# Kernel tuning notes

Measured on AMD Instinct MI355X. Metric: run time of the kernel, lower is better.

The kernel has to match this reference:

```python
import jax, jax.numpy as jnp
import numpy as np

EMBED_DIM = 1024
ATTN_DIM = 256
B, NQ, NK = 16, 1, 4096


def setup_inputs() -> dict:
    key = jax.random.key(0)
    ks = jax.random.split(key, 7)
    return {
        "q": jax.random.normal(ks[0], (B, NQ, EMBED_DIM), dtype=jnp.float32),
        "k": jax.random.normal(ks[1], (B, NK, EMBED_DIM), dtype=jnp.float32),
        "v": jax.random.normal(ks[2], (B, NK, EMBED_DIM), dtype=jnp.float32),
        "W_kq": jax.random.normal(ks[3], (EMBED_DIM, ATTN_DIM), dtype=jnp.float32) * (1.0 / np.sqrt(EMBED_DIM)),
        "b_kq": jax.random.normal(ks[4], (ATTN_DIM,), dtype=jnp.float32) * 0.02,
        "W_v": jax.random.normal(ks[5], (EMBED_DIM, EMBED_DIM), dtype=jnp.float32) * (1.0 / np.sqrt(EMBED_DIM)),
        "b_v": jax.random.normal(ks[6], (EMBED_DIM,), dtype=jnp.float32) * 0.02,
    }


def reference(q, k, v, W_kq, b_kq, W_v, b_v):
    # Shared kq projection applied to both q and k (embedding_dim -> attention_dim)
    qp = jnp.einsum("bqd,da->bqa", q, W_kq) + b_kq          # [B, NQ, A]
    kp = jnp.einsum("bkd,da->bka", k, W_kq) + b_kq          # [B, NK, A]
    vp = jnp.einsum("bkd,de->bke", v, W_v) + b_v            # [B, NK, E]
    # scores = q @ k^T / sqrt(attention_dim)  (k.shape[2] after projection)
    scores = jnp.einsum("bqa,bka->bqk", qp, kp) / jnp.sqrt(
        jnp.asarray(kp.shape[2], dtype=qp.dtype))
    attn = jax.nn.softmax(scores, axis=2)                   # [B, NQ, NK]
    out = jnp.einsum("bqk,bke->bqe", attn, vp)              # [B, NQ, E]
    return out.squeeze(1)                                   # [B, E] since NQ == 1
```

## Files before the change

### kernel.cpp

```cpp
#include <hip/hip_runtime.h>

#define ED 1024
#define AD 256
#define BB 16
#define NK 4096
#define NCH 64
#define KCH (NK/NCH)

#define OFF_QP    0
#define OFF_T     4096
#define OFF_WSUM  20480
#define OFF_PART  21504
#define OFF_OV    1070080
#define OFF_OPART 1086464

__global__ void k_qp(const float* __restrict__ q, const float* __restrict__ Wkq,
                     const float* __restrict__ bkq, float* __restrict__ qp) {
    int b = blockIdx.x, cg = blockIdx.y, tid = threadIdx.x;
    int c = cg * 64 + (tid & 63), dg = tid >> 6;
    __shared__ float qsh[ED];
    ((float4*)qsh)[tid] = ((const float4*)(q + b * ED))[tid];
    __syncthreads();
    float acc = 0.f;
    #pragma unroll 8
    for (int d = dg; d < ED; d += 4) acc += qsh[d] * Wkq[(size_t)d * AD + c];
    __shared__ float red[4][64];
    red[dg][tid & 63] = acc;
    __syncthreads();
    if (tid < 64) {
        float s = red[0][tid] + red[1][tid] + red[2][tid] + red[3][tid];
        qp[b * AD + cg * 64 + tid] = s + bkq[cg * 64 + tid];
    }
}

__global__ void k_t(const float* __restrict__ Wkq, const float* __restrict__ qp,
                    float* __restrict__ t) {
    int b = blockIdx.y, dbase = blockIdx.x * 128;
    int tid = threadIdx.x, wave = tid >> 6, lane = tid & 63;
    float4 qv = ((const float4*)(qp + b * AD))[lane];
    for (int r = 0; r < 16; ++r) {
        int d1 = dbase + wave * 32 + r;
        int d2 = d1 + 16;
        float4 w1 = ((const float4*)(Wkq + (size_t)d1 * AD))[lane];
        float4 w2 = ((const float4*)(Wkq + (size_t)d2 * AD))[lane];
        float s1 = w1.x*qv.x + w1.y*qv.y + w1.z*qv.z + w1.w*qv.w;
        float s2 = w2.x*qv.x + w2.y*qv.y + w2.z*qv.z + w2.w*qv.w;
        #pragma unroll
        for (int off = 32; off; off >>= 1) {
            s1 += __shfl_down(s1, off, 64);
            s2 += __shfl_down(s2, off, 64);
        }
        if (lane == 0) { t[b * ED + d1] = s1; t[b * ED + d2] = s2; }
    }
}

__global__ void k_fused(const float* __restrict__ k, const float* __restrict__ v,
                        const float* __restrict__ t, float* __restrict__ partial,
                        float* __restrict__ wsum) {
    int ch = blockIdx.x, b = blockIdx.y;
    int tid = threadIdx.x, wave = tid >> 6, lane = tid & 63;
    const float4* tb = (const float4*)(t + b * ED);
    float4 t0 = tb[lane], t1 = tb[64 + lane], t2 = tb[128 + lane], t3 = tb[192 + lane];
    __shared__ float ash[KCH];
    int row0 = ch * KCH + wave * 16;
    for (int r = 0; r < 8; ++r) {
        const float4* ka = (const float4*)(k + ((size_t)b * NK + row0 + r) * ED);
        const float4* kb = (const float4*)(k + ((size_t)b * NK + row0 + r + 8) * ED);
        float4 a0 = ka[lane], a1 = ka[64 + lane], a2 = ka[128 + lane], a3 = ka[192 + lane];
        float4 b0 = kb[lane], b1 = kb[64 + lane], b2 = kb[128 + lane], b3 = kb[192 + lane];
        float sa = a0.x*t0.x + a0.y*t0.y + a0.z*t0.z + a0.w*t0.w
                 + a1.x*t1.x + a1.y*t1.y + a1.z*t1.z + a1.w*t1.w
                 + a2.x*t2.x + a2.y*t2.y + a2.z*t2.z + a2.w*t2.w
                 + a3.x*t3.x + a3.y*t3.y + a3.z*t3.z + a3.w*t3.w;
        float sb = b0.x*t0.x + b0.y*t0.y + b0.z*t0.z + b0.w*t0.w
                 + b1.x*t1.x + b1.y*t1.y + b1.z*t1.z + b1.w*t1.w
                 + b2.x*t2.x + b2.y*t2.y + b2.z*t2.z + b2.w*t2.w
                 + b3.x*t3.x + b3.y*t3.y + b3.z*t3.z + b3.w*t3.w;
        #pragma unroll
        for (int off = 32; off; off >>= 1) {
            sa += __shfl_down(sa, off, 64);
            sb += __shfl_down(sb, off, 64);
        }
        if (lane == 0) {
            ash[wave * 16 + r]     = __expf(sa * 0.0625f);
            ash[wave * 16 + r + 8] = __expf(sb * 0.0625f);
        }
    }
    __syncthreads();
    if (tid < KCH) {
        float s = ash[tid];
        #pragma unroll
        for (int off = 32; off; off >>= 1) s += __shfl_down(s, off, 64);
        if (tid == 0) wsum[b * NCH + ch] = s;
    }
    const float4* vb = (const float4*)(v + ((size_t)b * NK + (size_t)ch * KCH) * ED);
    float4 acc = {0.f, 0.f, 0.f, 0.f};
    #pragma unroll 8
    for (int kk = 0; kk < KCH; ++kk) {
        float wt = ash[kk];
        float4 vv = vb[(size_t)kk * (ED / 4) + tid];
        acc.x += wt * vv.x; acc.y += wt * vv.y; acc.z += wt * vv.z; acc.w += wt * vv.w;
    }
    ((float4*)partial)[((size_t)(b * NCH + ch)) * (ED / 4) + tid] = acc;
}

__global__ void k_reduce(const float* __restrict__ partial, const float* __restrict__ wsum,
                         float* __restrict__ ov) {
    int b = blockIdx.x, dq = blockIdx.y, tid = threadIdx.x;
    int chg = tid >> 6, c = tid & 63;
    __shared__ float lsh;
    if (tid < 64) {
        float s = wsum[b * NCH + tid];
        #pragma unroll
        for (int off = 32; off; off >>= 1) s += __shfl_down(s, off, 64);
        if (tid == 0) lsh = s;
    }
    const float4* pb = (const float4*)(partial + (size_t)b * NCH * ED);
    float4 s4 = {0.f, 0.f, 0.f, 0.f};
    #pragma unroll 8
    for (int ch = chg; ch < NCH; ch += 4) {
        float4 p = pb[(size_t)ch * (ED / 4) + dq * 64 + c];
        s4.x += p.x; s4.y += p.y; s4.z += p.z; s4.w += p.w;
    }
    __shared__ float4 red[4][64];
    red[chg][c] = s4;
    __syncthreads();
    if (tid < 64) {
        float4 a0 = red[0][tid], a1 = red[1][tid], a2 = red[2][tid], a3 = red[3][tid];
        float linv = 1.0f / lsh;
        float4 r;
        r.x = (a0.x + a1.x + a2.x + a3.x) * linv;
        r.y = (a0.y + a1.y + a2.y + a3.y) * linv;
        r.z = (a0.z + a1.z + a2.z + a3.z) * linv;
        r.w = (a0.w + a1.w + a2.w + a3.w) * linv;
        ((float4*)(ov + b * ED + dq * 256))[tid] = r;
    }
}

__global__ void k_out(const float* __restrict__ ov, const float* __restrict__ Wv,
                      float* __restrict__ opart) {
    int cb = blockIdx.x, dq = blockIdx.y, tid = threadIdx.x;
    int col = cb * 64 + (tid & 63), dg = tid >> 6;
    __shared__ float ovsh[BB][256];
    for (int i = tid; i < BB * 64; i += 256) {
        int bb = i >> 6, c4 = i & 63;
        ((float4*)ovsh[bb])[c4] = ((const float4*)(ov + bb * ED + dq * 256))[c4];
    }
    __syncthreads();
    float acc[BB];
    #pragma unroll
    for (int b = 0; b < BB; ++b) acc[b] = 0.f;
    #pragma unroll 8
    for (int it = 0; it < 64; ++it) {
        int dd = dg + it * 4;
        float w = Wv[(size_t)(dq * 256 + dd) * ED + col];
        #pragma unroll
        for (int b = 0; b < BB; ++b) acc[b] += ovsh[b][dd] * w;
    }
    __shared__ float red[BB][256];
    #pragma unroll
    for (int b = 0; b < BB; ++b) red[b][tid] = acc[b];
    __syncthreads();
    int bgrp = tid >> 6, c = tid & 63;
    #pragma unroll
    for (int bi = 0; bi < 4; ++bi) {
        int b = bgrp * 4 + bi;
        float s = red[b][c] + red[b][64 + c] + red[b][128 + c] + red[b][192 + c];
        opart[((size_t)(dq * BB + b)) * ED + cb * 64 + c] = s;
    }
}

__global__ void k_final(const float* __restrict__ opart, const float* __restrict__ bv,
                        float* __restrict__ out) {
    int b = blockIdx.x, tid = threadIdx.x;
    float4 s = ((const float4*)(opart + (size_t)(0 * BB + b) * ED))[tid];
    #pragma unroll
    for (int dq = 1; dq < 4; ++dq) {
        float4 p = ((const float4*)(opart + (size_t)(dq * BB + b) * ED))[tid];
        s.x += p.x; s.y += p.y; s.z += p.z; s.w += p.w;
    }
    float4 bb = ((const float4*)bv)[tid];
    s.x += bb.x; s.y += bb.y; s.z += bb.z; s.w += bb.w;
    ((float4*)(out + b * ED))[tid] = s;
}

extern "C" void kernel_launch(void* const* d_in, const int* in_sizes, int n_in,
                              void* d_out, int out_size, void* d_ws, size_t ws_size,
                              hipStream_t stream) {
    const float* q   = (const float*)d_in[0];
    const float* k   = (const float*)d_in[1];
    const float* v   = (const float*)d_in[2];
    const float* Wkq = (const float*)d_in[3];
    const float* bkq = (const float*)d_in[4];
    const float* Wv  = (const float*)d_in[5];
    const float* bv  = (const float*)d_in[6];
    float* out = (float*)d_out;
    float* ws  = (float*)d_ws;

    float* qp      = ws + OFF_QP;
    float* t       = ws + OFF_T;
    float* wsum    = ws + OFF_WSUM;
    float* partial = ws + OFF_PART;
    float* ov      = ws + OFF_OV;
    float* opart   = ws + OFF_OPART;

    k_qp    <<<dim3(16, 4),   256, 0, stream>>>(q, Wkq, bkq, qp);
    k_t     <<<dim3(8, 16),   256, 0, stream>>>(Wkq, qp, t);
    k_fused <<<dim3(NCH, BB), 256, 0, stream>>>(k, v, t, partial, wsum);
    k_reduce<<<dim3(16, 4),   256, 0, stream>>>(partial, wsum, ov);
    k_out   <<<dim3(16, 4),   256, 0, stream>>>(ov, Wv, opart);
    k_final <<<16,            256, 0, stream>>>(opart, bv, out);
}
```

Baseline: 175.3 us.

## Stream K and V rows together per wave with register accumulation and LDS reduction

The fused score/value kernel now has each wave read a K row and the matching V row in the same iteration. It computes the score with an xor-shuffle allreduce so every lane holds the weight, then accumulates w*V into per-wave float4 registers. The separate phase that scored all K rows before streaming V is removed, so V loads no longer wait on a block-wide barrier and the two streams can overlap. Per-wave partial sums are combined through a 16KB LDS buffer at the end, which adds register pressure and shared memory that may reduce occupancy.

```diff
diff --git a/kernel.cpp b/kernel.cpp
--- a/kernel.cpp
+++ b/kernel.cpp
@@ -61,47 +61,46 @@
     int tid = threadIdx.x, wave = tid >> 6, lane = tid & 63;
     const float4* tb = (const float4*)(t + b * ED);
     float4 t0 = tb[lane], t1 = tb[64 + lane], t2 = tb[128 + lane], t3 = tb[192 + lane];
-    __shared__ float ash[KCH];
     int row0 = ch * KCH + wave * 16;
-    for (int r = 0; r < 8; ++r) {
-        const float4* ka = (const float4*)(k + ((size_t)b * NK + row0 + r) * ED);
-        const float4* kb = (const float4*)(k + ((size_t)b * NK + row0 + r + 8) * ED);
-        float4 a0 = ka[lane], a1 = ka[64 + lane], a2 = ka[128 + lane], a3 = ka[192 + lane];
-        float4 b0 = kb[lane], b1 = kb[64 + lane], b2 = kb[128 + lane], b3 = kb[192 + lane];
-        float sa = a0.x*t0.x + a0.y*t0.y + a0.z*t0.z + a0.w*t0.w
-                 + a1.x*t1.x + a1.y*t1.y + a1.z*t1.z + a1.w*t1.w
-                 + a2.x*t2.x + a2.y*t2.y + a2.z*t2.z + a2.w*t2.w
-                 + a3.x*t3.x + a3.y*t3.y + a3.z*t3.z + a3.w*t3.w;
-        float sb = b0.x*t0.x + b0.y*t0.y + b0.z*t0.z + b0.w*t0.w
-                 + b1.x*t1.x + b1.y*t1.y + b1.z*t1.z + b1.w*t1.w
-                 + b2.x*t2.x + b2.y*t2.y + b2.z*t2.z + b2.w*t2.w
-                 + b3.x*t3.x + b3.y*t3.y + b3.z*t3.z + b3.w*t3.w;
-        #pragma unroll
-        for (int off = 32; off; off >>= 1) {
-            sa += __shfl_down(sa, off, 64);
-            sb += __shfl_down(sb, off, 64);
-        }
-        if (lane == 0) {
-            ash[wave * 16 + r]     = __expf(sa * 0.0625f);
-            ash[wave * 16 + r + 8] = __expf(sb * 0.0625f);
-        }
-    }
-    __syncthreads();
-    if (tid < KCH) {
-        float s = ash[tid];
-        #pragma unroll
-        for (int off = 32; off; off >>= 1) s += __shfl_down(s, off, 64);
-        if (tid == 0) wsum[b * NCH + ch] = s;
-    }
-    const float4* vb = (const float4*)(v + ((size_t)b * NK + (size_t)ch * KCH) * ED);
-    float4 acc = {0.f, 0.f, 0.f, 0.f};
-    #pragma unroll 8
-    for (int kk = 0; kk < KCH; ++kk) {
-        float wt = ash[kk];
-        float4 vv = vb[(size_t)kk * (ED / 4) + tid];
-        acc.x += wt * vv.x; acc.y += wt * vv.y; acc.z += wt * vv.z; acc.w += wt * vv.w;
-    }
-    ((float4*)partial)[((size_t)(b * NCH + ch)) * (ED / 4) + tid] = acc;
+    const float4* kbase = (const float4*)(k + ((size_t)b * NK + row0) * ED);
+    const float4* vbase = (const float4*)(v + ((size_t)b * NK + row0) * ED);
+    float4 acc0 = {0,0,0,0}, acc1 = {0,0,0,0}, acc2 = {0,0,0,0}, acc3 = {0,0,0,0};
+    float wacc = 0.f;
+    #pragma unroll 2
+    for (int r = 0; r < 16; ++r) {
+        const float4* kr = kbase + (size_t)r * (ED / 4);
+        const float4* vr = vbase + (size_t)r * (ED / 4);
+        float4 k0 = kr[lane], k1 = kr[64 + lane], k2 = kr[128 + lane], k3 = kr[192 + lane];
+        float4 v0 = vr[lane], v1 = vr[64 + lane], v2 = vr[128 + lane], v3 = vr[192 + lane];
+        float s = k0.x*t0.x + k0.y*t0.y + k0.z*t0.z + k0.w*t0.w
+                + k1.x*t1.x + k1.y*t1.y + k1.z*t1.z + k1.w*t1.w
+                + k2.x*t2.x + k2.y*t2.y + k2.z*t2.z + k2.w*t2.w
+                + k3.x*t3.x + k3.y*t3.y + k3.z*t3.z + k3.w*t3.w;
+        #pragma unroll
+        for (int m = 32; m; m >>= 1) s += __shfl_xor(s, m, 64);
+        float w = __expf(s * 0.0625f);
+        wacc += w;
+        acc0.x += w*v0.x; acc0.y += w*v0.y; acc0.z += w*v0.z; acc0.w += w*v0.w;
+        acc1.x += w*v1.x; acc1.y += w*v1.y; acc1.z += w*v1.z; acc1.w += w*v1.w;
+        acc2.x += w*v2.x; acc2.y += w*v2.y; acc2.z += w*v2.z; acc2.w += w*v2.w;
+        acc3.x += w*v3.x; acc3.y += w*v3.y; acc3.z += w*v3.z; acc3.w += w*v3.w;
+    }
+    __shared__ float4 red[4][256];
+    red[wave][lane]       = acc0;
+    red[wave][64 + lane]  = acc1;
+    red[wave][128 + lane] = acc2;
+    red[wave][192 + lane] = acc3;
+    __shared__ float wred[4];
+    if (lane == 0) wred[wave] = wacc;
+    __syncthreads();
+    float4 a0 = red[0][tid], a1 = red[1][tid], a2 = red[2][tid], a3 = red[3][tid];
+    float4 r4;
+    r4.x = a0.x + a1.x + a2.x + a3.x;
+    r4.y = a0.y + a1.y + a2.y + a3.y;
+    r4.z = a0.z + a1.z + a2.z + a3.z;
+    r4.w = a0.w + a1.w + a2.w + a3.w;
+    ((float4*)partial)[((size_t)(b * NCH + ch)) * (ED / 4) + tid] = r4;
+    if (tid == 0) wsum[b * NCH + ch] = wred[0] + wred[1] + wred[2] + wred[3];
 }
 
 __global__ void k_reduce(const float* __restrict__ partial, const float* __restrict__ wsum,
```

After: 171.9 us (median of 2 runs). -2.0%, faster.

## Split fused attention kernel into separate scores and PV kernels with finer row blocks

Applied to the files above, without the earlier changes.

Splits the fused score+weighted-V kernel into a scores kernel that writes unnormalized exp weights and a PV kernel. Each now uses 16-row blocks, so the grid grows from 1024 to 4096 blocks. The larger partial buffer is reduced in two stages. The aim is better memory-level parallelism while streaming K and V. In exchange it adds an extra launch and extra partial-sum traffic.

```diff
diff --git a/kernel.cpp b/kernel.cpp
--- a/kernel.cpp
+++ b/kernel.cpp
@@ -4,15 +4,17 @@
 #define AD 256
 #define BB 16
 #define NK 4096
-#define NCH 64
-#define KCH (NK/NCH)
+#define RPB 16
+#define NBLK (BB * NK / RPB)
 
 #define OFF_QP    0
 #define OFF_T     4096
-#define OFF_WSUM  20480
-#define OFF_PART  21504
-#define OFF_OV    1070080
-#define OFF_OPART 1086464
+#define OFF_W     20480
+#define OFF_WSP   86016
+#define OFF_PART  90112
+#define OFF_PART2 4284416
+#define OFF_OV    4546560
+#define OFF_OPART 4562944
 
 __global__ void k_qp(const float* __restrict__ q, const float* __restrict__ Wkq,
                      const float* __restrict__ bkq, float* __restrict__ qp) {
@@ -54,87 +56,106 @@
     }
 }
 
-__global__ void k_fused(const float* __restrict__ k, const float* __restrict__ v,
-                        const float* __restrict__ t, float* __restrict__ partial,
-                        float* __restrict__ wsum) {
-    int ch = blockIdx.x, b = blockIdx.y;
+__global__ __launch_bounds__(256, 4)
+void k_scores(const float* __restrict__ k, const float* __restrict__ t,
+              float* __restrict__ w, float* __restrict__ wsumPart) {
+    int bid = blockIdx.x;
+    int b = bid >> 8, ch = bid & 255;
     int tid = threadIdx.x, wave = tid >> 6, lane = tid & 63;
     const float4* tb = (const float4*)(t + b * ED);
     float4 t0 = tb[lane], t1 = tb[64 + lane], t2 = tb[128 + lane], t3 = tb[192 + lane];
-    __shared__ float ash[KCH];
-    int row0 = ch * KCH + wave * 16;
-    for (int r = 0; r < 8; ++r) {
-        const float4* ka = (const float4*)(k + ((size_t)b * NK + row0 + r) * ED);
-        const float4* kb = (const float4*)(k + ((size_t)b * NK + row0 + r + 8) * ED);
+    int row0 = ch * RPB + wave * 4;
+    __shared__ float wsh[RPB];
+    #pragma unroll
+    for (int pr = 0; pr < 2; ++pr) {
+        int rA = row0 + pr * 2, rB = rA + 1;
+        const float4* ka = (const float4*)(k + ((size_t)b * NK + rA) * ED);
+        const float4* kb = (const float4*)(k + ((size_t)b * NK + rB) * ED);
         float4 a0 = ka[lane], a1 = ka[64 + lane], a2 = ka[128 + lane], a3 = ka[192 + lane];
-        float4 b0 = kb[lane], b1 = kb[64 + lane], b2 = kb[128 + lane], b3 = kb[192 + lane];
-        float sa = a0.x*t0.x + a0.y*t0.y + a0.z*t0.z + a0.w*t0.w
+        float4 c0 = kb[lane], c1 = kb[64 + lane], c2 = kb[128 + lane], c3 = kb[192 + lane];
+        float sA = a0.x*t0.x + a0.y*t0.y + a0.z*t0.z + a0.w*t0.w
                  + a1.x*t1.x + a1.y*t1.y + a1.z*t1.z + a1.w*t1.w
                  + a2.x*t2.x + a2.y*t2.y + a2.z*t2.z + a2.w*t2.w
                  + a3.x*t3.x + a3.y*t3.y + a3.z*t3.z + a3.w*t3.w;
-        float sb = b0.x*t0.x + b0.y*t0.y + b0.z*t0.z + b0.w*t0.w
-                 + b1.x*t1.x + b1.y*t1.y + b1.z*t1.z + b1.w*t1.w
-                 + b2.x*t2.x + b2.y*t2.y + b2.z*t2.z + b2.w*t2.w
-                 + b3.x*t3.x + b3.y*t3.y + b3.z*t3.z + b3.w*t3.w;
+        float sB = c0.x*t0.x + c0.y*t0.y + c0.z*t0.z + c0.w*t0.w
+                 + c1.x*t1.x + c1.y*t1.y + c1.z*t1.z + c1.w*t1.w
+                 + c2.x*t2.x + c2.y*t2.y + c2.z*t2.z + c2.w*t2.w
+                 + c3.x*t3.x + c3.y*t3.y + c3.z*t3.z + c3.w*t3.w;
         #pragma unroll
-        for (int off = 32; off; off >>= 1) {
-            sa += __shfl_down(sa, off, 64);
-            sb += __shfl_down(sb, off, 64);
+        for (int m = 32; m; m >>= 1) {
+            sA += __shfl_xor(sA, m, 64);
+            sB += __shfl_xor(sB, m, 64);
         }
         if (lane == 0) {
-            ash[wave * 16 + r]     = __expf(sa * 0.0625f);
-            ash[wave * 16 + r + 8] = __expf(sb * 0.0625f);
+            float wA = __expf(sA * 0.0625f), wB = __expf(sB * 0.0625f);
+            w[b * NK + rA] = wA;
+            w[b * NK + rB] = wB;
+            wsh[wave * 4 + pr * 2]     = wA;
+            wsh[wave * 4 + pr * 2 + 1] = wB;
         }
     }
     __syncthreads();
-    if (tid < KCH) {
-        float s = ash[tid];
-        #pragma unroll
-        for (int off = 32; off; off >>= 1) s += __shfl_down(s, off, 64);
-        if (tid == 0) wsum[b * NCH + ch] = s;
-    }
-    const float4* vb = (const float4*)(v + ((size_t)b * NK + (size_t)ch * KCH) * ED);
+    if (wave == 0) {
+        float s = (lane < RPB) ? wsh[lane] : 0.f;
+        s += __shfl_xor(s, 8, 64);
+        s += __shfl_xor(s, 4, 64);
+        s += __shfl_xor(s, 2, 64);
+        s += __shfl_xor(s, 1, 64);
+        if (lane == 0) wsumPart[bid] = s;
+    }
+}
+
+__global__ __launch_bounds__(256, 4)
+void k_pv(const float* __restrict__ v, const float* __restrict__ w,
+          float* __restrict__ partial) {
+    int bid = blockIdx.x;
+    int b = bid >> 8, ch = bid & 255;
+    int tid = threadIdx.x;
+    __shared__ float wsh[RPB];
+    if (tid < RPB) wsh[tid] = w[b * NK + ch * RPB + tid];
+    __syncthreads();
+    const float4* vb = (const float4*)(v + ((size_t)b * NK + (size_t)ch * RPB) * ED);
     float4 acc = {0.f, 0.f, 0.f, 0.f};
-    #pragma unroll 8
-    for (int kk = 0; kk < KCH; ++kk) {
-        float wt = ash[kk];
-        float4 vv = vb[(size_t)kk * (ED / 4) + tid];
+    #pragma unroll
+    for (int r = 0; r < RPB; ++r) {
+        float wt = wsh[r];
+        float4 vv = vb[(size_t)r * (ED / 4) + tid];
         acc.x += wt * vv.x; acc.y += wt * vv.y; acc.z += wt * vv.z; acc.w += wt * vv.w;
     }
-    ((float4*)partial)[((size_t)(b * NCH + ch)) * (ED / 4) + tid] = acc;
-}
-
-__global__ void k_reduce(const float* __restrict__ partial, const float* __restrict__ wsum,
-                         float* __restrict__ ov) {
-    int b = blockIdx.x, dq = blockIdx.y, tid = threadIdx.x;
-    int chg = tid >> 6, c = tid & 63;
-    __shared__ float lsh;
-    if (tid < 64) {
-        float s = wsum[b * NCH + tid];
-        #pragma unroll
-        for (int off = 32; off; off >>= 1) s += __shfl_down(s, off, 64);
-        if (tid == 0) lsh = s;
-    }
-    const float4* pb = (const float4*)(partial + (size_t)b * NCH * ED);
-    float4 s4 = {0.f, 0.f, 0.f, 0.f};
-    #pragma unroll 8
-    for (int ch = chg; ch < NCH; ch += 4) {
-        float4 p = pb[(size_t)ch * (ED / 4) + dq * 64 + c];
-        s4.x += p.x; s4.y += p.y; s4.z += p.z; s4.w += p.w;
-    }
-    __shared__ float4 red[4][64];
-    red[chg][c] = s4;
-    __syncthreads();
-    if (tid < 64) {
-        float4 a0 = red[0][tid], a1 = red[1][tid], a2 = red[2][tid], a3 = red[3][tid];
-        float linv = 1.0f / lsh;
-        float4 r;
-        r.x = (a0.x + a1.x + a2.x + a3.x) * linv;
-        r.y = (a0.y + a1.y + a2.y + a3.y) * linv;
-        r.z = (a0.z + a1.z + a2.z + a3.z) * linv;
-        r.w = (a0.w + a1.w + a2.w + a3.w) * linv;
-        ((float4*)(ov + b * ED + dq * 256))[tid] = r;
-    }
+    ((float4*)partial)[(size_t)bid * (ED / 4) + tid] = acc;
+}
+
+__global__ void k_reduce1(const float* __restrict__ partial, float* __restrict__ partial2) {
+    int b = blockIdx.x, g = blockIdx.y, tid = threadIdx.x;
+    const float4* pb = (const float4*)partial + ((size_t)((b << 8) + g * 16)) * (ED / 4);
+    float4 s = {0.f, 0.f, 0.f, 0.f};
+    #pragma unroll
+    for (int i = 0; i < 16; ++i) {
+        float4 p = pb[(size_t)i * (ED / 4) + tid];
+        s.x += p.x; s.y += p.y; s.z += p.z; s.w += p.w;
+    }
+    ((float4*)partial2)[((size_t)(b * 16 + g)) * (ED / 4) + tid] = s;
+}
+
+__global__ void k_reduce2(const float* __restrict__ partial2, const float* __restrict__ wsumPart,
+                          float* __restrict__ ov) {
+    int b = blockIdx.x, tid = threadIdx.x;
+    __shared__ float red[256];
+    red[tid] = wsumPart[b * 256 + tid];
+    __syncthreads();
+    for (int off = 128; off; off >>= 1) {
+        if (tid < off) red[tid] += red[tid + off];
+        __syncthreads();
+    }
+    float linv = 1.0f / red[0];
+    float4 s = {0.f, 0.f, 0.f, 0.f};
+    #pragma unroll
+    for (int g = 0; g < 16; ++g) {
+        float4 p = ((const float4*)partial2)[((size_t)(b * 16 + g)) * (ED / 4) + tid];
+        s.x += p.x; s.y += p.y; s.z += p.z; s.w += p.w;
+    }
+    s.x *= linv; s.y *= linv; s.z *= linv; s.w *= linv;
+    ((float4*)(ov + b * ED))[tid] = s;
 }
 
 __global__ void k_out(const float* __restrict__ ov, const float* __restrict__ Wv,
@@ -199,15 +220,19 @@
 
     float* qp      = ws + OFF_QP;
     float* t       = ws + OFF_T;
-    float* wsum    = ws + OFF_WSUM;
+    float* w       = ws + OFF_W;
+    float* wsp     = ws + OFF_WSP;
     float* partial = ws + OFF_PART;
+    float* part2   = ws + OFF_PART2;
     float* ov      = ws + OFF_OV;
     float* opart   = ws + OFF_OPART;
 
-    k_qp    <<<dim3(16, 4),   256, 0, stream>>>(q, Wkq, bkq, qp);
-    k_t     <<<dim3(8, 16),   256, 0, stream>>>(Wkq, qp, t);
-    k_fused <<<dim3(NCH, BB), 256, 0, stream>>>(k, v, t, partial, wsum);
-    k_reduce<<<dim3(16, 4),   256, 0, stream>>>(partial, wsum, ov);
-    k_out   <<<dim3(16, 4),   256, 0, stream>>>(ov, Wv, opart);
-    k_final <<<16,            256, 0, stream>>>(opart, bv, out);
-}
+    k_qp     <<<dim3(16, 4),  256, 0, stream>>>(q, Wkq, bkq, qp);
+    k_t      <<<dim3(8, 16),  256, 0, stream>>>(Wkq, qp, t);
+    k_scores <<<NBLK,         256, 0, stream>>>(k, t, w, wsp);
+    k_pv     <<<NBLK,         256, 0, stream>>>(v, w, partial);
+    k_reduce1<<<dim3(16, 16), 256, 0, stream>>>(partial, part2);
+    k_reduce2<<<16,           256, 0, stream>>>(part2, wsp, ov);
+    k_out    <<<dim3(16, 4),  256, 0, stream>>>(ov, Wv, opart);
+    k_final  <<<16,           256, 0, stream>>>(opart, bv, out);
+}
```

After: 179.6 us. +2.4%, slower.
